# Kernel tuning notes

Hardware: AMD Instinct MI355X
Metric: run time of the kernel (lower is better)

Reference implementation:

```python
import jax, jax.numpy as jnp
import numpy as np

N_NODES = 50000


def gcn_conv(x, edge_index, W, b):
    # PyG GCNConv: h = X @ W; add self-loops; sym-normalize; scatter-add to target; + bias
    N = x.shape[0]
    h = x @ W
    src = jnp.concatenate([edge_index[0], jnp.arange(N)])
    dst = jnp.concatenate([edge_index[1], jnp.arange(N)])
    ew = jnp.ones(src.shape[0], dtype=h.dtype)
    deg = jax.ops.segment_sum(ew, dst, num_segments=N)
    dinv = jnp.where(deg > 0, deg ** -0.5, 0.0)
    norm = dinv[src] * ew * dinv[dst]              # [E+N]
    msg = h[src] * norm[:, None]                   # gather + scale
    out = jax.ops.segment_sum(msg, dst, num_segments=N)  # scatter-add
    return out + b


def setup_inputs() -> dict:
    key = jax.random.key(0)
    ks = jax.random.split(key, 8)
    x = jax.random.normal(ks[0], (N_NODES, 128), dtype=jnp.float32)
    edge_index = jax.random.randint(ks[1], (2, 800000), 0, N_NODES)
    W1 = jax.random.normal(ks[2], (128, 96), dtype=jnp.float32) * 0.1
    b1 = jax.random.normal(ks[3], (96,), dtype=jnp.float32) * 0.1
    W_mu = jax.random.normal(ks[4], (96, 64), dtype=jnp.float32) * 0.1
    b_mu = jax.random.normal(ks[5], (64,), dtype=jnp.float32) * 0.1
    W_lv = jax.random.normal(ks[6], (96, 64), dtype=jnp.float32) * 0.1
    b_lv = jax.random.normal(ks[7], (64,), dtype=jnp.float32) * 0.1
    return {"x": x, "edge_index": edge_index, "W1": W1, "b1": b1,
            "W_mu": W_mu, "b_mu": b_mu, "W_lv": W_lv, "b_lv": b_lv}


def reference(x, edge_index, W1, b1, W_mu, b_mu, W_lv, b_lv):
    h = jax.nn.relu(gcn_conv(x, edge_index, W1, b1))
    mu = gcn_conv(h, edge_index, W_mu, b_mu).sum(axis=0, keepdims=True)      # SumAggregation -> [1, out]
    logvar = gcn_conv(h, edge_index, W_lv, b_lv).sum(axis=0, keepdims=True)  # [1, out]
    return (mu, logvar)
```

## Files before the change

kernel.cpp:

```cpp
#include <hip/hip_runtime.h>
#include <hip/hip_fp16.h>


#define NTHREADS 256
#define NCHUNK 32
#define LOG_NCHUNK 5
#define NSLICE 8
#define SLICE_MAX 6272
#define SORT_T 1024

__device__ inline void fma4(float4& c, float a, const float4& b) {
    c.x = fmaf(a, b.x, c.x); c.y = fmaf(a, b.y, c.y);
    c.z = fmaf(a, b.z, c.z); c.w = fmaf(a, b.w, c.w);
}

__device__ inline unsigned f2h(float a, float b) {
    __half2 h = __floats2half2_rn(a, b);
    return *reinterpret_cast<unsigned*>(&h);
}
__device__ inline float2 h2f(unsigned u) {
    __half2 h = *reinterpret_cast<__half2*>(&u);
    return __half22float2(h);
}

__launch_bounds__(SORT_T)
__global__ void k_count(const int* __restrict__ dst, int* __restrict__ partial,
                        int N, int E, int chunkE, int sliceN) {
    int c = blockIdx.x & (NCHUNK - 1), s = blockIdx.x >> LOG_NCHUNK;
    int nbase = s * sliceN;
    __shared__ int hist[SLICE_MAX];
    for (int j = threadIdx.x; j < sliceN; j += SORT_T) hist[j] = 0;
    __syncthreads();
    int e0 = c * chunkE, e1 = min(e0 + chunkE, E);
    int ne = e1 - e0;
    const int4* d4 = (const int4*)(dst + e0);
    int n4 = ne >> 2;
    for (int i = threadIdx.x; i < n4; i += SORT_T) {
        int4 d = d4[i];
        unsigned q;
        q = (unsigned)(d.x - nbase); if (q < (unsigned)sliceN) atomicAdd(&hist[q], 1);
        q = (unsigned)(d.y - nbase); if (q < (unsigned)sliceN) atomicAdd(&hist[q], 1);
        q = (unsigned)(d.z - nbase); if (q < (unsigned)sliceN) atomicAdd(&hist[q], 1);
        q = (unsigned)(d.w - nbase); if (q < (unsigned)sliceN) atomicAdd(&hist[q], 1);
    }
    if (threadIdx.x < (ne & 3)) {
        int d = dst[e0 + (n4 << 2) + threadIdx.x];
        unsigned q = (unsigned)(d - nbase);
        if (q < (unsigned)sliceN) atomicAdd(&hist[q], 1);
    }
    __syncthreads();
    for (int j = threadIdx.x; j < sliceN; j += SORT_T) {
        int n = nbase + j;
        if (n < N) partial[(size_t)c * N + n] = hist[j];
    }
}

__launch_bounds__(256)
__global__ void k_degdinv(const int* __restrict__ partial, int* __restrict__ deg,
                          float* __restrict__ dinv, int* __restrict__ blocksum, int N) {
    int tid = threadIdx.x;
    int n = blockIdx.x * 256 + tid;
    int s = 0;
    if (n < N) {
        #pragma unroll
        for (int c = 0; c < NCHUNK; ++c) s += partial[(size_t)c * N + n];
        deg[n] = s;
        dinv[n] = rsqrtf((float)(s + 1));
    }
    __shared__ int sh[256];
    sh[tid] = s;
    __syncthreads();
    #pragma unroll
    for (int off = 128; off; off >>= 1) {
        if (tid < off) sh[tid] += sh[tid + off];
        __syncthreads();
    }
    if (tid == 0) blocksum[blockIdx.x] = sh[0];
}

__global__ void k_bscan(const int* __restrict__ blocksum, int* __restrict__ blockoff,
                        int* __restrict__ rowptrN, int nb) {
    __shared__ int sh[256];
    int tid = threadIdx.x;
    int v = (tid < nb) ? blocksum[tid] : 0;
    sh[tid] = v;
    __syncthreads();
    for (int off = 1; off < 256; off <<= 1) {
        int t = (tid >= off) ? sh[tid - off] : 0;
        __syncthreads();
        sh[tid] += t;
        __syncthreads();
    }
    if (tid < nb) blockoff[tid] = sh[tid] - v;
    if (tid == nb - 1) *rowptrN = sh[tid];
}

__launch_bounds__(256)
__global__ void k_offs(int* __restrict__ partial, const int* __restrict__ deg,
                       const int* __restrict__ blockoff, int* __restrict__ rowptr, int N) {
    int tid = threadIdx.x;
    int n = blockIdx.x * 256 + tid;
    int v = (n < N) ? deg[n] : 0;
    __shared__ int sh[256];
    sh[tid] = v;
    __syncthreads();
    for (int off = 1; off < 256; off <<= 1) {
        int t = (tid >= off) ? sh[tid - off] : 0;
        __syncthreads();
        sh[tid] += t;
        __syncthreads();
    }
    int run = blockoff[blockIdx.x] + sh[tid] - v;
    if (n < N) {
        rowptr[n] = run;
        #pragma unroll
        for (int c = 0; c < NCHUNK; ++c) {
            size_t ix = (size_t)c * N + n;
            int t = partial[ix];
            partial[ix] = run;
            run += t;
        }
    }
}

__launch_bounds__(SORT_T)
__global__ void k_place(const int* __restrict__ src, const int* __restrict__ dst,
                        const float* __restrict__ dinv, int* __restrict__ offs,
                        int* __restrict__ col, int N, int E, int chunkE, int sliceN) {
    int c = blockIdx.x & (NCHUNK - 1), s = blockIdx.x >> LOG_NCHUNK;
    int nbase = s * sliceN;
    __shared__ int cur[SLICE_MAX];
    __shared__ float rs[SLICE_MAX];
    for (int j = threadIdx.x; j < sliceN; j += SORT_T) {
        int n = nbase + j;
        cur[j] = (n < N) ? offs[(size_t)c * N + n] : 0;
        rs[j] = 0.f;
    }
    __syncthreads();
    int e0 = c * chunkE, e1 = min(e0 + chunkE, E);
    int ne = e1 - e0;
    const int4* s4 = (const int4*)(src + e0);
    const int4* d4 = (const int4*)(dst + e0);
    int n4 = ne >> 2;
    for (int i = threadIdx.x; i < n4; i += SORT_T) {
        int4 sv = s4[i];
        int4 dv = d4[i];
        unsigned qd, qs;
        qd = (unsigned)(dv.x - nbase);
        if (qd < (unsigned)sliceN) { int p = atomicAdd(&cur[qd], 1); col[p] = sv.x; }
        qs = (unsigned)(sv.x - nbase);
        if (qs < (unsigned)sliceN) atomicAdd(&rs[qs], dinv[dv.x]);
        qd = (unsigned)(dv.y - nbase);
        if (qd < (unsigned)sliceN) { int p = atomicAdd(&cur[qd], 1); col[p] = sv.y; }
        qs = (unsigned)(sv.y - nbase);
        if (qs < (unsigned)sliceN) atomicAdd(&rs[qs], dinv[dv.y]);
        qd = (unsigned)(dv.z - nbase);
        if (qd < (unsigned)sliceN) { int p = atomicAdd(&cur[qd], 1); col[p] = sv.z; }
        qs = (unsigned)(sv.z - nbase);
        if (qs < (unsigned)sliceN) atomicAdd(&rs[qs], dinv[dv.z]);
        qd = (unsigned)(dv.w - nbase);
        if (qd < (unsigned)sliceN) { int p = atomicAdd(&cur[qd], 1); col[p] = sv.w; }
        qs = (unsigned)(sv.w - nbase);
        if (qs < (unsigned)sliceN) atomicAdd(&rs[qs], dinv[dv.w]);
    }
    if (threadIdx.x < (ne & 3)) {
        int e = e0 + (n4 << 2) + threadIdx.x;
        int sv = src[e], dv = dst[e];
        unsigned qd = (unsigned)(dv - nbase);
        if (qd < (unsigned)sliceN) { int p = atomicAdd(&cur[qd], 1); col[p] = sv; }
        unsigned qs = (unsigned)(sv - nbase);
        if (qs < (unsigned)sliceN) atomicAdd(&rs[qs], dinv[dv]);
    }
    __syncthreads();
    float* prs = (float*)offs;
    for (int j = threadIdx.x; j < sliceN; j += SORT_T) {
        int n = nbase + j;
        if (n < N) prs[(size_t)c * N + n] = rs[j];
    }
}

__launch_bounds__(256)
__global__ void k_gemm(const float* __restrict__ x, const float* __restrict__ W1,
                       const float* __restrict__ dinv, const float* __restrict__ prs,
                       float* __restrict__ cfac, __half* __restrict__ g, int n) {
    __shared__ float Ws[128 * 96];
    int tid = threadIdx.x;
    {
        const float4* wsrc = (const float4*)W1;
        float4* wdst = (float4*)Ws;
        #pragma unroll
        for (int i = 0; i < 12; ++i) wdst[tid + 256 * i] = wsrc[tid + 256 * i];
    }
    {
        int r = blockIdx.x * 128 + tid;
        if (tid < 128 && r < n) {
            float s = 0.f;
            #pragma unroll
            for (int c = 0; c < NCHUNK; ++c) s += prs[(size_t)c * n + r];
            float dv = dinv[r];
            cfac[r] = dv * (dv + s);
        }
    }
    __syncthreads();

    int tx = tid & 7;
    int ty = tid >> 3;
    int rbase = blockIdx.x * 128 + ty * 4;
    const float4* xp[4];
    bool vr[4];
    #pragma unroll
    for (int i = 0; i < 4; ++i) {
        int r = rbase + i;
        vr[i] = r < n;
        xp[i] = (const float4*)(x + (size_t)(vr[i] ? r : 0) * 128);
    }

    float4 acc[4][3];
    #pragma unroll
    for (int i = 0; i < 4; ++i)
        #pragma unroll
        for (int j = 0; j < 3; ++j) acc[i][j] = make_float4(0.f, 0.f, 0.f, 0.f);

    #pragma unroll 2
    for (int k4 = 0; k4 < 32; ++k4) {
        float4 a0 = xp[0][k4];
        float4 a1 = xp[1][k4];
        float4 a2 = xp[2][k4];
        float4 a3 = xp[3][k4];
        #pragma unroll
        for (int kk = 0; kk < 4; ++kk) {
            const float* wrow = &Ws[(k4 * 4 + kk) * 96 + tx * 12];
            float4 b0 = *(const float4*)(wrow);
            float4 b1 = *(const float4*)(wrow + 4);
            float4 b2 = *(const float4*)(wrow + 8);
            float av0 = (kk == 0) ? a0.x : (kk == 1) ? a0.y : (kk == 2) ? a0.z : a0.w;
            float av1 = (kk == 0) ? a1.x : (kk == 1) ? a1.y : (kk == 2) ? a1.z : a1.w;
            float av2 = (kk == 0) ? a2.x : (kk == 1) ? a2.y : (kk == 2) ? a2.z : a2.w;
            float av3 = (kk == 0) ? a3.x : (kk == 1) ? a3.y : (kk == 2) ? a3.z : a3.w;
            fma4(acc[0][0], av0, b0); fma4(acc[0][1], av0, b1); fma4(acc[0][2], av0, b2);
            fma4(acc[1][0], av1, b0); fma4(acc[1][1], av1, b1); fma4(acc[1][2], av1, b2);
            fma4(acc[2][0], av2, b0); fma4(acc[2][1], av2, b1); fma4(acc[2][2], av2, b2);
            fma4(acc[3][0], av3, b0); fma4(acc[3][1], av3, b1); fma4(acc[3][2], av3, b2);
        }
    }

    #pragma unroll
    for (int i = 0; i < 4; ++i) {
        if (!vr[i]) continue;
        int r = rbase + i;
        float dv = dinv[r];
        uint2* o = (uint2*)(g + (size_t)r * 96) + tx * 3;
        float4 t;
        t = acc[i][0]; o[0] = make_uint2(f2h(t.x * dv, t.y * dv), f2h(t.z * dv, t.w * dv));
        t = acc[i][1]; o[1] = make_uint2(f2h(t.x * dv, t.y * dv), f2h(t.z * dv, t.w * dv));
        t = acc[i][2]; o[2] = make_uint2(f2h(t.x * dv, t.y * dv), f2h(t.z * dv, t.w * dv));
    }
}

#define AGG_NODES 16
#define AGG_T (AGG_NODES * 24)
__launch_bounds__(AGG_T)
__global__ void k_agg(const uint2* __restrict__ g2, const int* __restrict__ col,
                      const int* __restrict__ rowptr, const float* __restrict__ dinv,
                      const float* __restrict__ cfac, const float* __restrict__ b1,
                      float* __restrict__ v_part, int n) {
    int tid = threadIdx.x;
    int nl = tid / 24;
    int ch = tid % 24;
    int d = blockIdx.x * AGG_NODES + nl;

    __shared__ float4 sh[AGG_NODES][24];

    float4 contrib = make_float4(0.f, 0.f, 0.f, 0.f);
    if (d < n) {
        float dd = dinv[d];
        int e0 = rowptr[d], e1 = rowptr[d + 1];
        float4 aA = make_float4(0.f, 0.f, 0.f, 0.f);
        float4 aB = make_float4(0.f, 0.f, 0.f, 0.f);
        int e = e0;
        for (; e + 4 <= e1; e += 4) {
            int s0 = col[e], s1 = col[e + 1], s2 = col[e + 2], s3 = col[e + 3];
            uint2 r0 = g2[(size_t)s0 * 24 + ch];
            uint2 r1 = g2[(size_t)s1 * 24 + ch];
            uint2 r2 = g2[(size_t)s2 * 24 + ch];
            uint2 r3 = g2[(size_t)s3 * 24 + ch];
            float2 f;
            f = h2f(r0.x); aA.x += f.x; aA.y += f.y;
            f = h2f(r0.y); aA.z += f.x; aA.w += f.y;
            f = h2f(r1.x); aB.x += f.x; aB.y += f.y;
            f = h2f(r1.y); aB.z += f.x; aB.w += f.y;
            f = h2f(r2.x); aA.x += f.x; aA.y += f.y;
            f = h2f(r2.y); aA.z += f.x; aA.w += f.y;
            f = h2f(r3.x); aB.x += f.x; aB.y += f.y;
            f = h2f(r3.y); aB.z += f.x; aB.w += f.y;
        }
        for (; e < e1; ++e) {
            uint2 r = g2[(size_t)col[e] * 24 + ch];
            float2 f;
            f = h2f(r.x); aA.x += f.x; aA.y += f.y;
            f = h2f(r.y); aA.z += f.x; aA.w += f.y;
        }
        uint2 rd = g2[(size_t)d * 24 + ch];
        float2 fd0 = h2f(rd.x), fd1 = h2f(rd.y);
        float4 b1c = ((const float4*)b1)[ch];
        float cd = cfac[d];
        float hx = fmaxf(fmaf(dd, aA.x + aB.x + fd0.x, b1c.x), 0.f);
        float hy = fmaxf(fmaf(dd, aA.y + aB.y + fd0.y, b1c.y), 0.f);
        float hz = fmaxf(fmaf(dd, aA.z + aB.z + fd1.x, b1c.z), 0.f);
        float hw = fmaxf(fmaf(dd, aA.w + aB.w + fd1.y, b1c.w), 0.f);
        contrib = make_float4(cd * hx, cd * hy, cd * hz, cd * hw);
    }
    sh[nl][ch] = contrib;
    __syncthreads();
    #pragma unroll
    for (int off = 8; off >= 1; off >>= 1) {
        if (nl < off) {
            float4 a = sh[nl][ch];
            float4 b = sh[nl + off][ch];
            a.x += b.x; a.y += b.y; a.z += b.z; a.w += b.w;
            sh[nl][ch] = a;
        }
        __syncthreads();
    }
    if (tid < 24) {
        ((float4*)(v_part + (size_t)blockIdx.x * 96))[tid] = sh[0][tid];
    }
}

__global__ void k_vred(const float* __restrict__ vp, float* __restrict__ v, int nb) {
    int j = blockIdx.x;
    float s = 0.f;
    for (int i = threadIdx.x; i < nb; i += 256) s += vp[(size_t)i * 96 + j];
    __shared__ float sh[256];
    sh[threadIdx.x] = s;
    __syncthreads();
    for (int off = 128; off; off >>= 1) {
        if (threadIdx.x < off) sh[threadIdx.x] += sh[threadIdx.x + off];
        __syncthreads();
    }
    if (threadIdx.x == 0) v[j] = sh[0];
}

__global__ void k_out(const float* __restrict__ v,
                      const float* __restrict__ Wmu, const float* __restrict__ bmu,
                      const float* __restrict__ Wlv, const float* __restrict__ blv,
                      float* __restrict__ out, float nN) {
    int tid = threadIdx.x;
    const float* W = (tid < 64) ? Wmu : Wlv;
    const float* b = (tid < 64) ? bmu : blv;
    int j = tid & 63;
    float s = 0.f;
    #pragma unroll
    for (int k = 0; k < 96; ++k) s = fmaf(v[k], W[k * 64 + j], s);
    out[tid] = s + nN * b[j];
}

extern "C" void kernel_launch(void* const* d_in, const int* in_sizes, int n_in,
                              void* d_out, int out_size, void* d_ws, size_t ws_size,
                              hipStream_t stream) {
    const float* x   = (const float*)d_in[0];
    const int*   ei  = (const int*)d_in[1];
    const float* W1  = (const float*)d_in[2];
    const float* b1  = (const float*)d_in[3];
    const float* Wmu = (const float*)d_in[4];
    const float* bmu = (const float*)d_in[5];
    const float* Wlv = (const float*)d_in[6];
    const float* blv = (const float*)d_in[7];
    float* out = (float*)d_out;

    const int N = in_sizes[0] / 128;
    const int E = in_sizes[1] / 2;
    const int* src = ei;
    const int* dst = ei + E;

    const int chunkE = (((E + NCHUNK - 1) / NCHUNK) + 3) & ~3;
    const int sliceN = (N + NSLICE - 1) / NSLICE;
    const int gN = (N + 255) / 256;

    size_t off = 0;
    auto alloc = [&](size_t bytes) -> char* {
        off = (off + 255) & ~(size_t)255;
        char* p = (char*)d_ws + off;
        off += bytes;
        return p;
    };
    int*    partial  = (int*)alloc((size_t)NCHUNK * N * 4);
    int*    rowptr   = (int*)alloc((size_t)(N + 1) * 4);
    int*    col      = (int*)alloc((size_t)E * 4);
    int*    deg      = (int*)alloc((size_t)N * 4);
    float*  dinv     = (float*)alloc((size_t)N * 4);
    float*  cfac     = (float*)alloc((size_t)N * 4);
    int*    blocksum = (int*)alloc((size_t)gN * 4);
    int*    blockoff = (int*)alloc((size_t)gN * 4);
    __half* g        = (__half*)alloc((size_t)N * 96 * 2);
    const int nAggBlocks = (N + AGG_NODES - 1) / AGG_NODES;
    float*  v_part   = (float*)alloc((size_t)nAggBlocks * 96 * 4);
    float*  v        = (float*)alloc(96 * 4);

    k_count<<<NCHUNK * NSLICE, SORT_T, 0, stream>>>(dst, partial, N, E, chunkE, sliceN);
    k_degdinv<<<gN, 256, 0, stream>>>(partial, deg, dinv, blocksum, N);
    k_bscan<<<1, 256, 0, stream>>>(blocksum, blockoff, rowptr + N, gN);
    k_offs<<<gN, 256, 0, stream>>>(partial, deg, blockoff, rowptr, N);
    k_place<<<NCHUNK * NSLICE, SORT_T, 0, stream>>>(src, dst, dinv, partial, col, N, E, chunkE, sliceN);
    k_gemm<<<(N + 127) / 128, 256, 0, stream>>>(x, W1, dinv, (const float*)partial, cfac, g, N);
    k_agg<<<nAggBlocks, AGG_T, 0, stream>>>((const uint2*)g, col, rowptr, dinv,
                                            cfac, b1, v_part, N);
    k_vred<<<96, 256, 0, stream>>>(v_part, v, nAggBlocks);
    k_out<<<1, 128, 0, stream>>>(v, Wmu, bmu, Wlv, blv, out, (float)N);
}
```

Measured before the change: 100.8 us.

## Store scaled features as fp8 and fold block-offset scan into k_offs

The per-node transformed features used by the gather-aggregate are stored as fp8 (scaled by 16) instead of fp16. This halves the bytes moved in the random-gather stage, and conversion uses the packed hardware fp8 instructions. Separately, the single-block k_bscan launch is removed: each k_offs block now sums the preceding block totals itself, and rowptr[N] is set to E. The fp8 format loses accuracy, which risks exceeding tolerance, and the redundant per-block reduction adds a little work.

```diff
diff --git a/kernel.cpp b/kernel.cpp
--- a/kernel.cpp
+++ b/kernel.cpp
@@ -9,18 +9,17 @@
 #define SLICE_MAX 6272
 #define SORT_T 1024
 
+typedef float v2f __attribute__((ext_vector_type(2)));
+
 __device__ inline void fma4(float4& c, float a, const float4& b) {
     c.x = fmaf(a, b.x, c.x); c.y = fmaf(a, b.y, c.y);
     c.z = fmaf(a, b.z, c.z); c.w = fmaf(a, b.w, c.w);
 }
 
-__device__ inline unsigned f2h(float a, float b) {
-    __half2 h = __floats2half2_rn(a, b);
-    return *reinterpret_cast<unsigned*>(&h);
-}
-__device__ inline float2 h2f(unsigned u) {
-    __half2 h = *reinterpret_cast<__half2*>(&u);
-    return __half22float2(h);
+__device__ inline unsigned pk_fp8(float a, float b, float c, float d) {
+    int p = __builtin_amdgcn_cvt_pk_fp8_f32(a, b, 0, false);
+    p = __builtin_amdgcn_cvt_pk_fp8_f32(c, d, p, true);
+    return (unsigned)p;
 }
 
 __launch_bounds__(SORT_T)
@@ -78,11 +77,24 @@
     if (tid == 0) blocksum[blockIdx.x] = sh[0];
 }
 
-__global__ void k_bscan(const int* __restrict__ blocksum, int* __restrict__ blockoff,
-                        int* __restrict__ rowptrN, int nb) {
+__launch_bounds__(256)
+__global__ void k_offs(int* __restrict__ partial, const int* __restrict__ deg,
+                       const int* __restrict__ blocksum, int* __restrict__ rowptr,
+                       int N, int E, int nb) {
+    int tid = threadIdx.x;
     __shared__ int sh[256];
-    int tid = threadIdx.x;
-    int v = (tid < nb) ? blocksum[tid] : 0;
+    int bs = (tid < nb && tid < (int)blockIdx.x) ? blocksum[tid] : 0;
+    sh[tid] = bs;
+    __syncthreads();
+    #pragma unroll
+    for (int off = 128; off; off >>= 1) {
+        if (tid < off) sh[tid] += sh[tid + off];
+        __syncthreads();
+    }
+    int blockoff = sh[0];
+    __syncthreads();
+    int n = blockIdx.x * 256 + tid;
+    int v = (n < N) ? deg[n] : 0;
     sh[tid] = v;
     __syncthreads();
     for (int off = 1; off < 256; off <<= 1) {
@@ -91,26 +103,7 @@
         sh[tid] += t;
         __syncthreads();
     }
-    if (tid < nb) blockoff[tid] = sh[tid] - v;
-    if (tid == nb - 1) *rowptrN = sh[tid];
-}
-
-__launch_bounds__(256)
-__global__ void k_offs(int* __restrict__ partial, const int* __restrict__ deg,
-                       const int* __restrict__ blockoff, int* __restrict__ rowptr, int N) {
-    int tid = threadIdx.x;
-    int n = blockIdx.x * 256 + tid;
-    int v = (n < N) ? deg[n] : 0;
-    __shared__ int sh[256];
-    sh[tid] = v;
-    __syncthreads();
-    for (int off = 1; off < 256; off <<= 1) {
-        int t = (tid >= off) ? sh[tid - off] : 0;
-        __syncthreads();
-        sh[tid] += t;
-        __syncthreads();
-    }
-    int run = blockoff[blockIdx.x] + sh[tid] - v;
+    int run = blockoff + sh[tid] - v;
     if (n < N) {
         rowptr[n] = run;
         #pragma unroll
@@ -121,6 +114,7 @@
             run += t;
         }
     }
+    if (blockIdx.x == 0 && tid == 0) rowptr[N] = E;
 }
 
 __launch_bounds__(SORT_T)
@@ -182,7 +176,7 @@
 __launch_bounds__(256)
 __global__ void k_gemm(const float* __restrict__ x, const float* __restrict__ W1,
                        const float* __restrict__ dinv, const float* __restrict__ prs,
-                       float* __restrict__ cfac, __half* __restrict__ g, int n) {
+                       float* __restrict__ cfac, unsigned* __restrict__ g, int n) {
     __shared__ float Ws[128 * 96];
     int tid = threadIdx.x;
     {
@@ -248,19 +242,19 @@
     for (int i = 0; i < 4; ++i) {
         if (!vr[i]) continue;
         int r = rbase + i;
-        float dv = dinv[r];
-        uint2* o = (uint2*)(g + (size_t)r * 96) + tx * 3;
+        float dv = dinv[r] * 16.f;
+        unsigned* o = g + (size_t)r * 24 + tx * 3;
         float4 t;
-        t = acc[i][0]; o[0] = make_uint2(f2h(t.x * dv, t.y * dv), f2h(t.z * dv, t.w * dv));
-        t = acc[i][1]; o[1] = make_uint2(f2h(t.x * dv, t.y * dv), f2h(t.z * dv, t.w * dv));
-        t = acc[i][2]; o[2] = make_uint2(f2h(t.x * dv, t.y * dv), f2h(t.z * dv, t.w * dv));
+        t = acc[i][0]; o[0] = pk_fp8(t.x * dv, t.y * dv, t.z * dv, t.w * dv);
+        t = acc[i][1]; o[1] = pk_fp8(t.x * dv, t.y * dv, t.z * dv, t.w * dv);
+        t = acc[i][2]; o[2] = pk_fp8(t.x * dv, t.y * dv, t.z * dv, t.w * dv);
     }
 }
 
 #define AGG_NODES 16
 #define AGG_T (AGG_NODES * 24)
 __launch_bounds__(AGG_T)
-__global__ void k_agg(const uint2* __restrict__ g2, const int* __restrict__ col,
+__global__ void k_agg(const unsigned* __restrict__ g1, const int* __restrict__ col,
                       const int* __restrict__ rowptr, const float* __restrict__ dinv,
                       const float* __restrict__ cfac, const float* __restrict__ b1,
                       float* __restrict__ v_part, int n) {
@@ -273,41 +267,45 @@
 
     float4 contrib = make_float4(0.f, 0.f, 0.f, 0.f);
     if (d < n) {
-        float dd = dinv[d];
+        float dds = dinv[d] * 0.0625f;
         int e0 = rowptr[d], e1 = rowptr[d + 1];
         float4 aA = make_float4(0.f, 0.f, 0.f, 0.f);
         float4 aB = make_float4(0.f, 0.f, 0.f, 0.f);
         int e = e0;
         for (; e + 4 <= e1; e += 4) {
             int s0 = col[e], s1 = col[e + 1], s2 = col[e + 2], s3 = col[e + 3];
-            uint2 r0 = g2[(size_t)s0 * 24 + ch];
-            uint2 r1 = g2[(size_t)s1 * 24 + ch];
-            uint2 r2 = g2[(size_t)s2 * 24 + ch];
-            uint2 r3 = g2[(size_t)s3 * 24 + ch];
-            float2 f;
-            f = h2f(r0.x); aA.x += f.x; aA.y += f.y;
-            f = h2f(r0.y); aA.z += f.x; aA.w += f.y;
-            f = h2f(r1.x); aB.x += f.x; aB.y += f.y;
-            f = h2f(r1.y); aB.z += f.x; aB.w += f.y;
-            f = h2f(r2.x); aA.x += f.x; aA.y += f.y;
-            f = h2f(r2.y); aA.z += f.x; aA.w += f.y;
-            f = h2f(r3.x); aB.x += f.x; aB.y += f.y;
-            f = h2f(r3.y); aB.z += f.x; aB.w += f.y;
+            unsigned u0 = g1[(size_t)s0 * 24 + ch];
+            unsigned u1 = g1[(size_t)s1 * 24 + ch];
+            unsigned u2 = g1[(size_t)s2 * 24 + ch];
+            unsigned u3 = g1[(size_t)s3 * 24 + ch];
+            v2f f;
+            f = __builtin_amdgcn_cvt_pk_f32_fp8(u0, false); aA.x += f.x; aA.y += f.y;
+            f = __builtin_amdgcn_cvt_pk_f32_fp8(u0, true);  aA.z += f.x; aA.w += f.y;
+            f = __builtin_amdgcn_cvt_pk_f32_fp8(u1, false); aB.x += f.x; aB.y += f.y;
+            f = __builtin_amdgcn_cvt_pk_f32_fp8(u1, true);  aB.z += f.x; aB.w += f.y;
+            f = __builtin_amdgcn_cvt_pk_f32_fp8(u2, false); aA.x += f.x; aA.y += f.y;
+            f = __builtin_amdgcn_cvt_pk_f32_fp8(u2, true);  aA.z += f.x; aA.w += f.y;
+            f = __builtin_amdgcn_cvt_pk_f32_fp8(u3, false); aB.x += f.x; aB.y += f.y;
+            f = __builtin_amdgcn_cvt_pk_f32_fp8(u3, true);  aB.z += f.x; aB.w += f.y;
         }
         for (; e < e1; ++e) {
-            uint2 r = g2[(size_t)col[e] * 24 + ch];
-            float2 f;
-            f = h2f(r.x); aA.x += f.x; aA.y += f.y;
-            f = h2f(r.y); aA.z += f.x; aA.w += f.y;
-        }
-        uint2 rd = g2[(size_t)d * 24 + ch];
-        float2 fd0 = h2f(rd.x), fd1 = h2f(rd.y);
+            unsigned u = g1[(size_t)col[e] * 24 + ch];
+            v2f f;
+            f = __builtin_amdgcn_cvt_pk_f32_fp8(u, false); aA.x += f.x; aA.y += f.y;
+            f = __builtin_amdgcn_cvt_pk_f32_fp8(u, true);  aA.z += f.x; aA.w += f.y;
+        }
+        {
+            unsigned u = g1[(size_t)d * 24 + ch];
+            v2f f;
+            f = __builtin_amdgcn_cvt_pk_f32_fp8(u, false); aA.x += f.x; aA.y += f.y;
+            f = __builtin_amdgcn_cvt_pk_f32_fp8(u, true);  aA.z += f.x; aA.w += f.y;
+        }
         float4 b1c = ((const float4*)b1)[ch];
         float cd = cfac[d];
-        float hx = fmaxf(fmaf(dd, aA.x + aB.x + fd0.x, b1c.x), 0.f);
-        float hy = fmaxf(fmaf(dd, aA.y + aB.y + fd0.y, b1c.y), 0.f);
-        float hz = fmaxf(fmaf(dd, aA.z + aB.z + fd1.x, b1c.z), 0.f);
-        float hw = fmaxf(fmaf(dd, aA.w + aB.w + fd1.y, b1c.w), 0.f);
+        float hx = fmaxf(fmaf(dds, aA.x + aB.x, b1c.x), 0.f);
+        float hy = fmaxf(fmaf(dds, aA.y + aB.y, b1c.y), 0.f);
+        float hz = fmaxf(fmaf(dds, aA.z + aB.z, b1c.z), 0.f);
+        float hw = fmaxf(fmaf(dds, aA.w + aB.w, b1c.w), 0.f);
         contrib = make_float4(cd * hx, cd * hy, cd * hz, cd * hw);
     }
     sh[nl][ch] = contrib;
@@ -384,27 +382,24 @@
         off += bytes;
         return p;
     };
-    int*    partial  = (int*)alloc((size_t)NCHUNK * N * 4);
-    int*    rowptr   = (int*)alloc((size_t)(N + 1) * 4);
-    int*    col      = (int*)alloc((size_t)E * 4);
-    int*    deg      = (int*)alloc((size_t)N * 4);
-    float*  dinv     = (float*)alloc((size_t)N * 4);
-    float*  cfac     = (float*)alloc((size_t)N * 4);
-    int*    blocksum = (int*)alloc((size_t)gN * 4);
-    int*    blockoff = (int*)alloc((size_t)gN * 4);
-    __half* g        = (__half*)alloc((size_t)N * 96 * 2);
+    int*      partial  = (int*)alloc((size_t)NCHUNK * N * 4);
+    int*      rowptr   = (int*)alloc((size_t)(N + 1) * 4);
+    int*      col      = (int*)alloc((size_t)E * 4);
+    int*      deg      = (int*)alloc((size_t)N * 4);
+    float*    dinv     = (float*)alloc((size_t)N * 4);
+    float*    cfac     = (float*)alloc((size_t)N * 4);
+    int*      blocksum = (int*)alloc((size_t)gN * 4);
+    unsigned* g        = (unsigned*)alloc((size_t)N * 96);
     const int nAggBlocks = (N + AGG_NODES - 1) / AGG_NODES;
-    float*  v_part   = (float*)alloc((size_t)nAggBlocks * 96 * 4);
-    float*  v        = (float*)alloc(96 * 4);
+    float*    v_part   = (float*)alloc((size_t)nAggBlocks * 96 * 4);
+    float*    v        = (float*)alloc(96 * 4);
 
     k_count<<<NCHUNK * NSLICE, SORT_T, 0, stream>>>(dst, partial, N, E, chunkE, sliceN);
     k_degdinv<<<gN, 256, 0, stream>>>(partial, deg, dinv, blocksum, N);
-    k_bscan<<<1, 256, 0, stream>>>(blocksum, blockoff, rowptr + N, gN);
-    k_offs<<<gN, 256, 0, stream>>>(partial, deg, blockoff, rowptr, N);
+    k_offs<<<gN, 256, 0, stream>>>(partial, deg, blocksum, rowptr, N, E, gN);
     k_place<<<NCHUNK * NSLICE, SORT_T, 0, stream>>>(src, dst, dinv, partial, col, N, E, chunkE, sliceN);
     k_gemm<<<(N + 127) / 128, 256, 0, stream>>>(x, W1, dinv, (const float*)partial, cfac, g, N);
-    k_agg<<<nAggBlocks, AGG_T, 0, stream>>>((const uint2*)g, col, rowptr, dinv,
-                                            cfac, b1, v_part, N);
+    k_agg<<<nAggBlocks, AGG_T, 0, stream>>>(g, col, rowptr, dinv, cfac, b1, v_part, N);
     k_vred<<<96, 256, 0, stream>>>(v_part, v, nAggBlocks);
     k_out<<<1, 128, 0, stream>>>(v, Wmu, bmu, Wlv, blv, out, (float)N);
 }
```

Result: faster. 92.81 us (-7.9%).
